# Kernel tuning notes

Measured on AMD Instinct MI355X. Metric: run time of the kernel, lower is better.

The kernel has to match this reference:

```python
import jax, jax.numpy as jnp
import numpy as np

B, LO, LQ = 4, 2048, 2048
NIN, H, G, NH = 41, 128, 10, 2


def _lin(key, din, dout):
    kw, kb = jax.random.split(key)
    W = jax.random.normal(kw, (din, dout), jnp.float32) / np.float32(np.sqrt(din))
    b = jax.random.normal(kb, (dout,), jnp.float32) * 0.01
    return W, b


def setup_inputs() -> dict:
    key = jax.random.key(0)
    ks = jax.random.split(key, 24)
    t_obs = jax.random.normal(ks[0], (B, LO, 1), jnp.float32)
    ch_obs = jax.random.randint(ks[1], (B, LO, 1), 0, NIN).astype(jnp.float32)
    v_obs = jax.random.normal(ks[2], (B, LO, 1), jnp.float32)
    obs = jnp.concatenate([t_obs, ch_obs, v_obs], -1)  # [B, LO, 3]
    t_q = jax.random.normal(ks[3], (B, LQ, 1), jnp.float32)
    ch_q = jax.random.randint(ks[4], (B, LQ, 1), 0, NIN).astype(jnp.float32)
    xq = jnp.concatenate([t_q, ch_q], -1)  # [B, LQ, 2]
    mobs = (jax.random.uniform(ks[5], (B, LO)) < 0.9).astype(jnp.float32)
    mq = (jax.random.uniform(ks[6], (B, LQ)) < 0.9).astype(jnp.float32)
    w_q0, b_q0 = _lin(ks[7], 1, 1)
    w_q1, b_q1 = _lin(ks[8], 1, H - 1)
    w_o0, b_o0 = _lin(ks[9], 1, 1)
    w_o1, b_o1 = _lin(ks[10], 1, H - 1)
    w_cobs, b_cobs = _lin(ks[11], NIN, H)
    w_cq, b_cq = _lin(ks[12], NIN, H)
    w_qp, b_qp = _lin(ks[13], 2 * H, H)
    w_kp, b_kp = _lin(ks[14], 2 * H + 1, H)
    ws_q, ws_qb = _lin(ks[15], H, H * NH)
    ws_o, ws_ob = _lin(ks[16], H * NH, H)
    ww_q, ww_qb = _lin(ks[17], H, H * NH)
    ww_o, ww_ob = _lin(ks[18], H * NH, H)
    wc_q, wc_qb = _lin(ks[19], H, H * NH)
    wc_o, wc_ob = _lin(ks[20], H * NH, H)
    w_split, b_split = _lin(ks[21], H, H * G)
    mix_wt = jax.random.normal(ks[22], (G, H), jnp.float32)
    w_mix, b_mix = _lin(ks[23], H, 1)
    return dict(obs=obs, mobs=mobs, xq=xq, mq=mq,
                w_q0=w_q0, b_q0=b_q0, w_q1=w_q1, b_q1=b_q1,
                w_o0=w_o0, b_o0=b_o0, w_o1=w_o1, b_o1=b_o1,
                w_cobs=w_cobs, b_cobs=b_cobs, w_cq=w_cq, b_cq=b_cq,
                w_qp=w_qp, b_qp=b_qp, w_kp=w_kp, b_kp=b_kp,
                ws_q=ws_q, ws_qb=ws_qb, ws_o=ws_o, ws_ob=ws_ob,
                ww_q=ww_q, ww_qb=ww_qb, ww_o=ww_o, ww_ob=ww_ob,
                wc_q=wc_q, wc_qb=wc_qb, wc_o=wc_o, wc_ob=wc_ob,
                w_split=w_split, b_split=b_split,
                mix_wt=mix_wt, w_mix=w_mix, b_mix=b_mix)


def _mha(q_in, k_in, v_in, mask, Wq, bq, Wo, bo):
    # Faithful to original: query_param projects q, k AND v (key/val params are unused).
    Bb, Lq, _ = q_in.shape
    Lk = k_in.shape[1]
    q = (q_in @ Wq + bq).reshape(Bb, Lq, NH, H)
    k = (k_in @ Wq + bq).reshape(Bb, Lk, NH, H)
    v = (v_in @ Wq + bq).reshape(Bb, Lk, NH, H)
    scores = jnp.einsum('bqhd,bkhd->bhqk', q, k) / np.float32(np.sqrt(H))
    scores = jnp.where(mask[:, None, :, :] == 0, jnp.float32(-1e6), scores)
    attn = jax.nn.softmax(scores, axis=-1)
    out = jnp.einsum('bhqk,bkhd->bqhd', attn, v).reshape(Bb, Lq, NH * H)
    return q_in + out @ Wo + bo


def _forward(obs, mobs, xq, mq,
             w_q0, b_q0, w_q1, b_q1, w_o0, b_o0, w_o1, b_o1,
             w_cobs, b_cobs, w_cq, b_cq, w_qp, b_qp, w_kp, b_kp,
             ws_q, ws_qb, ws_o, ws_ob, ww_q, ww_qb, ww_o, ww_ob,
             wc_q, wc_qb, wc_o, wc_ob, w_split, b_split,
             mix_wt, w_mix, b_mix):
    cq = xq[:, :, 1]
    tq = xq[:, :, 0:1]
    cobs = obs[:, :, 1]
    tobs = obs[:, :, 0:1]
    xobs = obs[:, :, 2:]
    tq = jnp.concatenate([tq @ w_q0 + b_q0, jnp.sin(tq @ w_q1 + b_q1)], -1)        # [B, LQ, H]
    tobs = jnp.concatenate([tobs @ w_o0 + b_o0, jnp.sin(tobs @ w_o1 + b_o1)], -1)  # [B, LO, H]
    cobs = jax.nn.one_hot(cobs.astype(jnp.int32), NIN, dtype=obs.dtype)
    cq = jax.nn.one_hot(cq.astype(jnp.int32), NIN, dtype=obs.dtype)
    cobs = jax.nn.relu(cobs @ w_cobs + b_cobs)
    cq = jax.nn.relu(cq @ w_cq + b_cq)
    obs_ = jnp.concatenate([tobs, cobs, xobs], -1) * mobs[:, :, None]  # [B, LO, 2H+1]
    xq_ = jnp.concatenate([tq, cq], -1) * mq[:, :, None]               # [B, LQ, 2H]
    qry_embed = xq_ @ w_qp + b_qp    # [B, LQ, H]
    obs_embed = obs_ @ w_kp + b_kp   # [B, LO, H]
    mask_self = mobs[:, :, None] * mobs[:, None, :]   # [B, LO, LO]
    mask_cross = mq[:, :, None] * mobs[:, None, :]    # [B, LQ, LO]
    mask_wts = jnp.broadcast_to(mobs[:, None, :], (obs.shape[0], G, mobs.shape[1]))  # [B, G, LO]
    wts_query = jnp.broadcast_to(mix_wt[None], (obs.shape[0], G, H))
    x = jax.nn.relu(_mha(obs_embed, obs_embed, obs_embed, mask_self, ws_q, ws_qb, ws_o, ws_ob))
    mw_ = _mha(wts_query, x, x, mask_wts, ww_q, ww_qb, ww_o, ww_ob)
    mw = jax.nn.softmax((mw_ @ w_mix + b_mix)[..., 0], axis=-1)  # [B, G]
    x = jax.nn.relu(_mha(qry_embed, x, x, mask_cross, wc_q, wc_qb, wc_o, wc_ob))
    x = (x @ w_split + b_split).reshape(x.shape[0], x.shape[1], G, H)
    return jnp.transpose(x, (0, 2, 1, 3)), mw  # ([B, G, LQ, H], [B, G])


def reference(obs, mobs, xq, mq,
              w_q0, b_q0, w_q1, b_q1, w_o0, b_o0, w_o1, b_o1,
              w_cobs, b_cobs, w_cq, b_cq, w_qp, b_qp, w_kp, b_kp,
              ws_q, ws_qb, ws_o, ws_ob, ww_q, ww_qb, ww_o, ww_ob,
              wc_q, wc_qb, wc_o, wc_ob, w_split, b_split,
              mix_wt, w_mix, b_mix):
    return _forward(obs, mobs, xq, mq,
                    w_q0, b_q0, w_q1, b_q1, w_o0, b_o0, w_o1, b_o1,
                    w_cobs, b_cobs, w_cq, b_cq, w_qp, b_qp, w_kp, b_kp,
                    ws_q, ws_qb, ws_o, ws_ob, ww_q, ww_qb, ww_o, ww_ob,
                    wc_q, wc_qb, wc_o, wc_ob, w_split, b_split,
                    mix_wt, w_mix, b_mix)
```

## Files before the change

### kernel.cpp

```cpp
#include <hip/hip_runtime.h>
#include <hip/hip_bf16.h>

#define B_  4
#define L_  2048
#define H_  128
#define NH_ 2
#define G_  10
#define NIN_ 41

typedef __hip_bfloat16 bf16;
typedef __attribute__((ext_vector_type(8))) short bf16x8s;
typedef __attribute__((ext_vector_type(4))) float f32x4;

__device__ __forceinline__ unsigned short f2bf_bits(float x) {
    __hip_bfloat16 h = __float2bfloat16(x);
    return *reinterpret_cast<unsigned short*>(&h);
}
__device__ __forceinline__ float us2f(unsigned short s) {
    return __uint_as_float(((unsigned int)s) << 16);
}

__global__ __launch_bounds__(128)
void featall_kernel(const float* __restrict__ xq, const float* __restrict__ mq,
                    const float* __restrict__ obs, const float* __restrict__ mobs,
                    const float* __restrict__ w_q0, const float* __restrict__ b_q0,
                    const float* __restrict__ w_q1, const float* __restrict__ b_q1,
                    const float* __restrict__ w_cq, const float* __restrict__ b_cq,
                    const float* __restrict__ w_o0, const float* __restrict__ b_o0,
                    const float* __restrict__ w_o1, const float* __restrict__ b_o1,
                    const float* __restrict__ w_cobs, const float* __restrict__ b_cobs,
                    bf16* __restrict__ featq, bf16* __restrict__ feato)
{
    const int blk = blockIdx.x;
    const int j   = threadIdx.x;
    const int NROW = B_ * L_;
    if (blk < NROW) {
        const int row = blk;
        const float t   = xq[row * 2 + 0];
        const float chf = xq[row * 2 + 1];
        int ch = (int)chf; ch = max(0, min(NIN_ - 1, ch));
        const float m   = mq[row];
        float tf;
        if (j == 0) tf = t * w_q0[0] + b_q0[0];
        else        tf = __sinf(t * w_q1[j - 1] + b_q1[j - 1]);
        float cf = fmaxf(w_cq[ch * H_ + j] + b_cq[j], 0.f);
        featq[(size_t)row * 256 + j]       = __float2bfloat16(tf * m);
        featq[(size_t)row * 256 + 128 + j] = __float2bfloat16(cf * m);
    } else {
        const int row = blk - NROW;
        const float t   = obs[row * 3 + 0];
        const float chf = obs[row * 3 + 1];
        const float xv  = obs[row * 3 + 2];
        int ch = (int)chf; ch = max(0, min(NIN_ - 1, ch));
        const float m   = mobs[row];
        float tf;
        if (j == 0) tf = t * w_o0[0] + b_o0[0];
        else        tf = __sinf(t * w_o1[j - 1] + b_o1[j - 1]);
        float cf = fmaxf(w_cobs[ch * H_ + j] + b_cobs[j], 0.f);
        bf16* r = feato + (size_t)row * 288;
        r[j]       = __float2bfloat16(tf * m);
        r[128 + j] = __float2bfloat16(cf * m);
        if (j == 0) r[256] = __float2bfloat16(xv * m);
        if (j < 31) r[257 + j] = __float2bfloat16(0.f);
    }
}

struct WtArgs {
    const float* W[8];
    bf16* T[8];
    int K[8], Kp[8], N[8];
};
__global__ __launch_bounds__(288)
void wtrans_all_kernel(WtArgs a)
{
    const int i = blockIdx.y, n = blockIdx.x, k = threadIdx.x;
    if (n >= a.N[i] || k >= a.Kp[i]) return;
    a.T[i][(size_t)n * a.Kp[i] + k] =
        (k < a.K[i]) ? __float2bfloat16(a.W[i][(size_t)k * a.N[i] + n])
                     : __float2bfloat16(0.f);
}

__global__ __launch_bounds__(256)
void kvtrans_kernel(const bf16* __restrict__ in, bf16* __restrict__ out)
{
    __shared__ unsigned short tile[64 * 136];
    const int tid = threadIdx.x;
    const int l0 = blockIdx.x * 64;
    const int bh = blockIdx.y;
    const unsigned short* src = (const unsigned short*)(in + (size_t)bh * L_ * H_);
    unsigned short* dst = (unsigned short*)(out + (size_t)bh * H_ * L_);
    #pragma unroll
    for (int p = 0; p < 4; p++) {
        const int l = p * 16 + (tid >> 4);
        const int d0 = (tid & 15) * 8;
        *(uint4*)&tile[l * 136 + d0] = *(const uint4*)&src[(size_t)(l0 + l) * H_ + d0];
    }
    __syncthreads();
    const int d  = tid >> 1;
    const int lh = (tid & 1) * 32;
    unsigned short buf[32];
    #pragma unroll
    for (int j = 0; j < 32; j++) buf[j] = tile[(lh + j) * 136 + d];
    #pragma unroll
    for (int j = 0; j < 4; j++)
        *(uint4*)&dst[(size_t)d * L_ + l0 + lh + j * 8] = *(uint4*)&buf[j * 8];
}

__global__ __launch_bounds__(128)
void gemm_kernel(const bf16* __restrict__ A, const bf16* __restrict__ WT,
                 const float* __restrict__ bias, const bf16* __restrict__ R,
                 void* __restrict__ out, int K, int N, int mode, int do_relu)
{
    const int wave = threadIdx.x >> 6, lane = threadIdx.x & 63;
    const int quad = lane >> 4, l15 = lane & 15;
    const int m0 = blockIdx.x * 32 + wave * 16;
    const int n0 = blockIdx.y * 64;

    f32x4 acc[4];
    #pragma unroll
    for (int c = 0; c < 4; c++) acc[c] = (f32x4){0.f, 0.f, 0.f, 0.f};

    const bf16* arow = A + (size_t)(m0 + l15) * K;
    #pragma unroll 4
    for (int kc = 0; kc < K; kc += 32) {
        bf16x8s af = *(const bf16x8s*)(arow + kc + quad * 8);
        #pragma unroll
        for (int c = 0; c < 4; c++) {
            bf16x8s wf = *(const bf16x8s*)(WT + (size_t)(n0 + c * 16 + l15) * K + kc + quad * 8);
            acc[c] = __builtin_amdgcn_mfma_f32_16x16x32_bf16(af, wf, acc[c], 0, 0, 0);
        }
    }

    #pragma unroll
    for (int c = 0; c < 4; c++) {
        const int n = n0 + c * 16 + l15;
        const float bv = bias[n];
        #pragma unroll
        for (int r = 0; r < 4; r++) {
            const int m = m0 + quad * 4 + r;
            float v = acc[c][r] + bv;
            if (R != nullptr) v += __bfloat162float(R[(size_t)m * N + n]);
            if (do_relu) v = fmaxf(v, 0.f);
            if (mode == 0) {
                ((float*)out)[(size_t)m * N + n] = v;
            } else if (mode == 1) {
                ((bf16*)out)[(size_t)m * N + n] = __float2bfloat16(v);
            } else if (mode == 2) {
                const int b = m >> 11, l = m & 2047, hh = n >> 7, d = n & 127;
                ((bf16*)out)[(((size_t)(b * NH_ + hh)) * L_ + l) * H_ + d] = __float2bfloat16(v);
            } else {
                const int b = m >> 11, q = m & 2047, g = n >> 7, hh = n & 127;
                ((float*)out)[(((size_t)(b * G_ + g)) * L_ + q) * H_ + hh] = v;
            }
        }
    }
}

#define KT_S 136
#define VT_S 72
#define PS_S 72

__global__ __launch_bounds__(512, 2)
void flash_attn_kernel(const bf16* __restrict__ Qb, const bf16* __restrict__ KVb,
                       const bf16* __restrict__ KVTb,
                       const float* __restrict__ mQ, const float* __restrict__ mK,
                       bf16* __restrict__ O)
{
    __shared__ __align__(16) char smem[90112];
    unsigned short* Ks = (unsigned short*)smem;
    unsigned short* Vs = (unsigned short*)(smem + 34816);
    unsigned short* Ps = (unsigned short*)(smem + 71680);
    float* Ocomb = (float*)smem;
    float* mcomb = (float*)(smem + 33792);
    float* lcomb = (float*)(smem + 34048);

    const int tid  = threadIdx.x;
    const int lane = tid & 63;
    const int wave = tid >> 6;
    const int half = wave >> 2;
    const int wq   = wave & 3;
    const int quad = lane >> 4;
    const int l15  = lane & 15;
    const int t256 = tid & 255;
    const int bh = blockIdx.x, b = bh >> 1, h = bh & 1;
    const int q0 = blockIdx.y * 64;

    const bf16* kvb = KVb  + (size_t)bh * L_ * H_;
    const bf16* kvt = KVTb + (size_t)bh * H_ * L_;
    const float* mkb = mK + b * L_;

    const bf16* qrow = Qb + ((size_t)bh * L_ + q0 + wq * 16 + l15) * H_;
    bf16x8s qf[4];
    #pragma unroll
    for (int kc = 0; kc < 4; kc++)
        qf[kc] = *(const bf16x8s*)(qrow + kc * 32 + quad * 8);

    bool qz[4];
    #pragma unroll
    for (int r = 0; r < 4; r++)
        qz[r] = (mQ != nullptr) && (mQ[b * L_ + q0 + wq * 16 + quad * 4 + r] == 0.f);

    float mo[4], li[4];
    f32x4 Oacc[8];
    #pragma unroll
    for (int r = 0; r < 4; r++) { mo[r] = -1e30f; li[r] = 0.f; }
    #pragma unroll
    for (int c = 0; c < 8; c++) Oacc[c] = (f32x4){0.f, 0.f, 0.f, 0.f};

    const float SCALE = 0.08838834764831845f;
    unsigned short* KsH = Ks + half * 64 * KT_S;
    unsigned short* VsH = Vs + half * 128 * VT_S;
    unsigned short* pw  = Ps + wave * 16 * PS_S;

    const int krow_b = t256 >> 4, kcol = (t256 & 15) * 8;
    const int vrow_b = t256 >> 3, vcol = (t256 & 7) * 8;

    uint4 rk[4], rv[4];
    const int ks0 = half * 1024;

    {
        const int kb = ks0;
        #pragma unroll
        for (int p = 0; p < 4; p++)
            rk[p] = *(const uint4*)(kvb + (size_t)(kb + p * 16 + krow_b) * H_ + kcol);
        #pragma unroll
        for (int p = 0; p < 4; p++)
            rv[p] = *(const uint4*)(kvt + (size_t)(p * 32 + vrow_b) * L_ + kb + vcol);
        #pragma unroll
        for (int p = 0; p < 4; p++)
            *(uint4*)&KsH[(p * 16 + krow_b) * KT_S + kcol] = rk[p];
        #pragma unroll
        for (int p = 0; p < 4; p++)
            *(uint4*)&VsH[(p * 32 + vrow_b) * VT_S + vcol] = rv[p];
    }
    __syncthreads();

    for (int it = 0; it < 16; it++) {
        const int kb = ks0 + it * 64;

        if (it + 1 < 16) {
            const int kn = kb + 64;
            #pragma unroll
            for (int p = 0; p < 4; p++)
                rk[p] = *(const uint4*)(kvb + (size_t)(kn + p * 16 + krow_b) * H_ + kcol);
            #pragma unroll
            for (int p = 0; p < 4; p++)
                rv[p] = *(const uint4*)(kvt + (size_t)(p * 32 + vrow_b) * L_ + kn + vcol);
        }

        float koff[4];
        #pragma unroll
        for (int t = 0; t < 4; t++)
            koff[t] = (mkb[kb + t * 16 + l15] != 0.f) ? 0.f : -1000000.f;

        f32x4 sa[4];
        #pragma unroll
        for (int t = 0; t < 4; t++) sa[t] = (f32x4){0.f, 0.f, 0.f, 0.f};
        #pragma unroll
        for (int t = 0; t < 4; t++)
            #pragma unroll
            for (int kc = 0; kc < 4; kc++) {
                bf16x8s kf = *(const bf16x8s*)&KsH[(t * 16 + l15) * KT_S + kc * 32 + quad * 8];
                sa[t] = __builtin_amdgcn_mfma_f32_16x16x32_bf16(qf[kc], kf, sa[t], 0, 0, 0);
            }

        float s[4][4], mx[4];
        #pragma unroll
        for (int r = 0; r < 4; r++) {
            #pragma unroll
            for (int t = 0; t < 4; t++) {
                const float v = sa[t][r] * SCALE + koff[t];
                s[t][r] = qz[r] ? -1000000.f : v;
            }
            mx[r] = fmaxf(fmaxf(s[0][r], s[1][r]), fmaxf(s[2][r], s[3][r]));
        }
        #pragma unroll
        for (int off = 1; off < 16; off <<= 1)
            #pragma unroll
            for (int r = 0; r < 4; r++) mx[r] = fmaxf(mx[r], __shfl_xor(mx[r], off));

        float al[4], rs[4];
        #pragma unroll
        for (int r = 0; r < 4; r++) {
            const float mn = fmaxf(mo[r], mx[r]);
            al[r] = __expf(mo[r] - mn);
            mo[r] = mn;
            rs[r] = 0.f;
        }
        #pragma unroll
        for (int t = 0; t < 4; t++)
            #pragma unroll
            for (int r = 0; r < 4; r++) {
                const float p = __expf(s[t][r] - mo[r]);
                rs[r] += p;
                pw[(quad * 4 + r) * PS_S + t * 16 + l15] = f2bf_bits(p);
            }
        #pragma unroll
        for (int off = 1; off < 16; off <<= 1)
            #pragma unroll
            for (int r = 0; r < 4; r++) rs[r] += __shfl_xor(rs[r], off);
        #pragma unroll
        for (int r = 0; r < 4; r++) li[r] = li[r] * al[r] + rs[r];
        #pragma unroll
        for (int c = 0; c < 8; c++)
            #pragma unroll
            for (int r = 0; r < 4; r++) Oacc[c][r] *= al[r];

        bf16x8s pf0 = *(bf16x8s*)&pw[l15 * PS_S + quad * 8];
        bf16x8s pf1 = *(bf16x8s*)&pw[l15 * PS_S + 32 + quad * 8];

        #pragma unroll
        for (int c = 0; c < 8; c++) {
            bf16x8s v0 = *(const bf16x8s*)&VsH[(c * 16 + l15) * VT_S + quad * 8];
            bf16x8s v1 = *(const bf16x8s*)&VsH[(c * 16 + l15) * VT_S + 32 + quad * 8];
            Oacc[c] = __builtin_amdgcn_mfma_f32_16x16x32_bf16(pf0, v0, Oacc[c], 0, 0, 0);
            Oacc[c] = __builtin_amdgcn_mfma_f32_16x16x32_bf16(pf1, v1, Oacc[c], 0, 0, 0);
        }

        __syncthreads();
        if (it + 1 < 16) {
            #pragma unroll
            for (int p = 0; p < 4; p++)
                *(uint4*)&KsH[(p * 16 + krow_b) * KT_S + kcol] = rk[p];
            #pragma unroll
            for (int p = 0; p < 4; p++)
                *(uint4*)&VsH[(p * 32 + vrow_b) * VT_S + vcol] = rv[p];
            __syncthreads();
        }
    }

    if (half == 1) {
        #pragma unroll
        for (int c = 0; c < 8; c++)
            #pragma unroll
            for (int r = 0; r < 4; r++)
                Ocomb[(size_t)(wq * 16 + quad * 4 + r) * 132 + c * 16 + l15] = Oacc[c][r];
        if (l15 == 0) {
            #pragma unroll
            for (int r = 0; r < 4; r++) {
                mcomb[wq * 16 + quad * 4 + r] = mo[r];
                lcomb[wq * 16 + quad * 4 + r] = li[r];
            }
        }
    }
    __syncthreads();
    if (half == 0) {
        bf16* orow = O + ((size_t)b * L_ + q0 + wq * 16) * (NH_ * H_) + h * H_;
        #pragma unroll
        for (int r = 0; r < 4; r++) {
            const int row = quad * 4 + r;
            const float m1 = mcomb[wq * 16 + row];
            const float l1 = lcomb[wq * 16 + row];
            const float M  = fmaxf(mo[r], m1);
            const float a0 = __expf(mo[r] - M);
            const float a1 = __expf(m1 - M);
            const float inv = 1.f / (a0 * li[r] + a1 * l1);
            #pragma unroll
            for (int c = 0; c < 8; c++)
                orow[(size_t)row * (NH_ * H_) + c * 16 + l15] =
                    __float2bfloat16((a0 * Oacc[c][r] +
                                      a1 * Ocomb[(size_t)(wq * 16 + row) * 132 + c * 16 + l15]) * inv);
        }
    }
}

__global__ __launch_bounds__(256)
void qmwb_kernel(const float* __restrict__ mixwt, const float* __restrict__ W,
                 const float* __restrict__ bias, bf16* __restrict__ qmwb)
{
    const int g = blockIdx.x;
    const int c = threadIdx.x;
    const int h = c >> 7, d = c & 127;
    if (g >= G_) { qmwb[((size_t)h * 16 + g) * 128 + d] = __float2bfloat16(0.f); return; }
    __shared__ float xr[128];
    if (c < 128) xr[c] = mixwt[g * 128 + c];
    __syncthreads();
    float acc = bias[c];
    #pragma unroll 8
    for (int i = 0; i < 128; i++)
        acc += xr[i] * W[i * 256 + c];
    qmwb[((size_t)h * 16 + g) * 128 + d] = __float2bfloat16(acc);
}

__global__ __launch_bounds__(256)
void mwpartial_kernel(const bf16* __restrict__ qmwb, const bf16* __restrict__ kvmw,
                      const float* __restrict__ mK,
                      float* __restrict__ mwO, float* __restrict__ mwM,
                      float* __restrict__ mwL)
{
    __shared__ __align__(16) unsigned short Ks[128 * 136];
    __shared__ float Qs[10 * 128];
    __shared__ float sc[10 * 128];
    __shared__ float mst[10], lst[10];

    const int tid = threadIdx.x;
    const int split = blockIdx.x, h = blockIdx.y, b = blockIdx.z;
    const int kbase = split * 128;
    const float SCALE = 0.08838834764831845f;

    for (int idx = tid; idx < 1280; idx += 256)
        Qs[idx] = __bfloat162float(qmwb[((size_t)h * 16 + (idx >> 7)) * 128 + (idx & 127)]);
    {
        const int rr = tid >> 1, half = tid & 1;
        const bf16* src = kvmw + (((size_t)(b * NH_ + h)) * L_ + kbase + rr) * H_ + half * 64;
        #pragma unroll
        for (int i = 0; i < 8; i++)
            *(uint4*)(&Ks[rr * 136 + half * 64 + i * 8]) = *(const uint4*)(src + i * 8);
    }
    __syncthreads();

    {
        const int j = tid & 127, qh = tid >> 7;
        float acc[5] = {0.f, 0.f, 0.f, 0.f, 0.f};
        for (int dc = 0; dc < 128; dc += 8) {
            bf16x8s kv = *(bf16x8s*)(&Ks[j * 136 + dc]);
            float kf[8];
            #pragma unroll
            for (int e = 0; e < 8; e++) kf[e] = us2f(((unsigned short*)&kv)[e]);
            #pragma unroll
            for (int qq = 0; qq < 5; qq++) {
                const float* Qrow = &Qs[(qh * 5 + qq) * 128 + dc];
                #pragma unroll
                for (int e = 0; e < 8; e++) acc[qq] += Qrow[e] * kf[e];
            }
        }
        const bool kz = (mK[b * L_ + kbase + j] == 0.f);
        #pragma unroll
        for (int qq = 0; qq < 5; qq++)
            sc[(qh * 5 + qq) * 128 + j] = kz ? -1000000.f : acc[qq] * SCALE;
    }
    __syncthreads();
    if (tid < 160) {
        const int q = tid >> 4, t16 = tid & 15;
        float m = -3.4e38f;
        for (int jj = t16; jj < 128; jj += 16) m = fmaxf(m, sc[q * 128 + jj]);
        #pragma unroll
        for (int off = 1; off < 16; off <<= 1) m = fmaxf(m, __shfl_xor(m, off));
        if (t16 == 0) mst[q] = m;
    }
    __syncthreads();
    {
        const int j = tid & 127, qh = tid >> 7;
        #pragma unroll
        for (int qq = 0; qq < 5; qq++) {
            const int idx = (qh * 5 + qq) * 128 + j;
            sc[idx] = __expf(sc[idx] - mst[qh * 5 + qq]);
        }
    }
    __syncthreads();
    if (tid < 160) {
        const int q = tid >> 4, t16 = tid & 15;
        float s = 0.f;
        for (int jj = t16; jj < 128; jj += 16) s += sc[q * 128 + jj];
        #pragma unroll
        for (int off = 1; off < 16; off <<= 1) s += __shfl_xor(s, off);
        if (t16 == 0) lst[q] = s;
    }
    __syncthreads();
    {
        const int d = tid & 127, qh = tid >> 7;
        float acc[5] = {0.f, 0.f, 0.f, 0.f, 0.f};
        for (int jj = 0; jj < 128; jj++) {
            const float v = us2f(Ks[jj * 136 + d]);
            #pragma unroll
            for (int qq = 0; qq < 5; qq++)
                acc[qq] += sc[(qh * 5 + qq) * 128 + jj] * v;
        }
        const size_t base = ((size_t)(b * NH_ + h) * 16 + split) * 10;
        #pragma unroll
        for (int qq = 0; qq < 5; qq++)
            mwO[(base + qh * 5 + qq) * 128 + d] = acc[qq];
    }
    if (tid < 10) {
        const size_t base = ((size_t)(b * NH_ + h) * 16 + split) * 10;
        mwM[base + tid] = mst[tid];
        mwL[base + tid] = lst[tid];
    }
}

__global__ __launch_bounds__(256)
void mwcombine_kernel(const float* __restrict__ mwO, const float* __restrict__ mwM,
                      const float* __restrict__ mwL, float* __restrict__ mwat)
{
    const int bg = blockIdx.x;
    const int b = bg / G_, q = bg % G_;
    const int h = threadIdx.x >> 7, d = threadIdx.x & 127;
    const size_t hb = (size_t)(b * NH_ + h) * 16;
    float M = -3.4e38f;
    for (int s = 0; s < 16; s++) M = fmaxf(M, mwM[(hb + s) * 10 + q]);
    float l = 0.f, o = 0.f;
    for (int s = 0; s < 16; s++) {
        const float a = __expf(mwM[(hb + s) * 10 + q] - M);
        l += a * mwL[(hb + s) * 10 + q];
        o += a * mwO[((hb + s) * 10 + q) * 128 + d];
    }
    mwat[(size_t)bg * 256 + h * 128 + d] = o / l;
}

__global__ __launch_bounds__(128)
void mwproj_kernel(const float* __restrict__ A, const float* __restrict__ mixwt,
                   const float* __restrict__ W, const float* __restrict__ bias,
                   float* __restrict__ Y)
{
    const int bg  = blockIdx.x;
    const int g   = bg % G_;
    const int tid = threadIdx.x;
    __shared__ float ar[256];
    ar[tid]       = A[(size_t)bg * 256 + tid];
    ar[tid + 128] = A[(size_t)bg * 256 + tid + 128];
    __syncthreads();
    float acc = mixwt[g * 128 + tid] + bias[tid];
    #pragma unroll 8
    for (int i = 0; i < 256; i++)
        acc += ar[i] * W[i * 128 + tid];
    Y[(size_t)bg * 128 + tid] = acc;
}

__global__ __launch_bounds__(64)
void mwfinal_kernel(const float* __restrict__ MW, const float* __restrict__ wmix,
                    const float* __restrict__ bmix, float* __restrict__ out)
{
    const int b = blockIdx.x;
    const int g = threadIdx.x;
    __shared__ float z[16];
    if (g < G_) {
        float acc = bmix[0];
        for (int i = 0; i < 128; i++)
            acc += MW[((size_t)b * G_ + g) * 128 + i] * wmix[i];
        z[g] = acc;
    }
    __syncthreads();
    if (g == 0) {
        float mx = -3.4e38f;
        for (int i = 0; i < G_; i++) mx = fmaxf(mx, z[i]);
        float e[G_]; float s = 0.f;
        for (int i = 0; i < G_; i++) { e[i] = __expf(z[i] - mx); s += e[i]; }
        for (int i = 0; i < G_; i++) out[b * G_ + i] = e[i] / s;
    }
}

extern "C" void kernel_launch(void* const* d_in, const int* in_sizes, int n_in,
                              void* d_out, int out_size, void* d_ws, size_t ws_size,
                              hipStream_t stream)
{
    const float* obs    = (const float*)d_in[0];
    const float* mobs   = (const float*)d_in[1];
    const float* xq     = (const float*)d_in[2];
    const float* mq     = (const float*)d_in[3];
    const float* w_q0   = (const float*)d_in[4];
    const float* b_q0   = (const float*)d_in[5];
    const float* w_q1   = (const float*)d_in[6];
    const float* b_q1   = (const float*)d_in[7];
    const float* w_o0   = (const float*)d_in[8];
    const float* b_o0   = (const float*)d_in[9];
    const float* w_o1   = (const float*)d_in[10];
    const float* b_o1   = (const float*)d_in[11];
    const float* w_cobs = (const float*)d_in[12];
    const float* b_cobs = (const float*)d_in[13];
    const float* w_cq   = (const float*)d_in[14];
    const float* b_cq   = (const float*)d_in[15];
    const float* w_qp   = (const float*)d_in[16];
    const float* b_qp   = (const float*)d_in[17];
    const float* w_kp   = (const float*)d_in[18];
    const float* b_kp   = (const float*)d_in[19];
    const float* ws_q   = (const float*)d_in[20];
    const float* ws_qb  = (const float*)d_in[21];
    const float* ws_o   = (const float*)d_in[22];
    const float* ws_ob  = (const float*)d_in[23];
    const float* ww_q   = (const float*)d_in[24];
    const float* ww_qb  = (const float*)d_in[25];
    const float* ww_o   = (const float*)d_in[26];
    const float* ww_ob  = (const float*)d_in[27];
    const float* wc_q   = (const float*)d_in[28];
    const float* wc_qb  = (const float*)d_in[29];
    const float* wc_o   = (const float*)d_in[30];
    const float* wc_ob  = (const float*)d_in[31];
    const float* w_split= (const float*)d_in[32];
    const float* b_split= (const float*)d_in[33];
    const float* mix_wt = (const float*)d_in[34];
    const float* w_mix  = (const float*)d_in[35];
    const float* b_mix  = (const float*)d_in[36];

    float* out = (float*)d_out;
    char* ws  = (char*)d_ws;

    const size_t MB = (size_t)1 << 20;
    const size_t KB = (size_t)1 << 10;
    if (ws_size < 31 * MB) return;

    const int NROW = B_ * L_;
    bf16* featq = (bf16*)(ws + 0);
    bf16* feato = (bf16*)(ws + 4 * MB);
    bf16* qe_bf = (bf16*)(ws + 8 * MB + 512 * KB);
    bf16* x_bf  = (bf16*)(ws + 10 * MB + 512 * KB);
    bf16* oe_bf = (bf16*)(ws + 12 * MB + 512 * KB);
    bf16* abuf  = (bf16*)(ws + 14 * MB + 512 * KB);
    bf16* x2_bf = (bf16*)(ws + 18 * MB + 512 * KB);
    bf16* kvmw  = (bf16*)(ws + 20 * MB + 512 * KB);
    bf16* kvT   = (bf16*)(ws + 24 * MB + 512 * KB);
    char* wbase = ws + 28 * MB + 512 * KB;
    bf16* wqpT  = (bf16*)(wbase + 0);
    bf16* wkpT  = (bf16*)(wbase + 64 * KB);
    bf16* wsqT  = (bf16*)(wbase + 136 * KB);
    bf16* wsoT  = (bf16*)(wbase + 200 * KB);
    bf16* wwqT  = (bf16*)(wbase + 264 * KB);
    bf16* wcqT  = (bf16*)(wbase + 328 * KB);
    bf16* wcoT  = (bf16*)(wbase + 392 * KB);
    bf16* wsplT = (bf16*)(wbase + 456 * KB);
    bf16* qmwb  = (bf16*)(wbase + 776 * KB);
    float* mwO  = (float*)(wbase + 784 * KB);
    float* mwM  = (float*)(wbase + 1424 * KB);
    float* mwL  = (float*)(wbase + 1432 * KB);
    float* mwat = (float*)(wbase + 1440 * KB);
    float* mw_  = (float*)(wbase + 1480 * KB);
    bf16* kvbs  = featq;
    bf16* qcb   = featq;
    bf16* kvcb  = (bf16*)(ws + 4 * MB);
    bf16* abuf2 = abuf;

    WtArgs wa;
    wa.W[0]=w_qp;   wa.T[0]=wqpT;  wa.K[0]=256; wa.Kp[0]=256; wa.N[0]=128;
    wa.W[1]=w_kp;   wa.T[1]=wkpT;  wa.K[1]=257; wa.Kp[1]=288; wa.N[1]=128;
    wa.W[2]=ws_q;   wa.T[2]=wsqT;  wa.K[2]=128; wa.Kp[2]=128; wa.N[2]=256;
    wa.W[3]=ws_o;   wa.T[3]=wsoT;  wa.K[3]=256; wa.Kp[3]=256; wa.N[3]=128;
    wa.W[4]=ww_q;   wa.T[4]=wwqT;  wa.K[4]=128; wa.Kp[4]=128; wa.N[4]=256;
    wa.W[5]=wc_q;   wa.T[5]=wcqT;  wa.K[5]=128; wa.Kp[5]=128; wa.N[5]=256;
    wa.W[6]=wc_o;   wa.T[6]=wcoT;  wa.K[6]=256; wa.Kp[6]=256; wa.N[6]=128;
    wa.W[7]=w_split;wa.T[7]=wsplT; wa.K[7]=128; wa.Kp[7]=128; wa.N[7]=1280;
    wtrans_all_kernel<<<dim3(1280, 8), 288, 0, stream>>>(wa);

    featall_kernel<<<2 * NROW, 128, 0, stream>>>(xq, mq, obs, mobs,
                                                 w_q0, b_q0, w_q1, b_q1, w_cq, b_cq,
                                                 w_o0, b_o0, w_o1, b_o1, w_cobs, b_cobs,
                                                 featq, feato);
    gemm_kernel<<<dim3(NROW/32, 2), 128, 0, stream>>>(featq, wqpT, b_qp, nullptr,
                                                      qe_bf, 256, 128, 1, 0);
    gemm_kernel<<<dim3(NROW/32, 2), 128, 0, stream>>>(feato, wkpT, b_kp, nullptr,
                                                      oe_bf, 288, 128, 1, 0);
    gemm_kernel<<<dim3(NROW/32, 4), 128, 0, stream>>>(oe_bf, wsqT, ws_qb, nullptr,
                                                      kvbs, 128, 256, 2, 0);
    kvtrans_kernel<<<dim3(L_/64, B_*NH_), 256, 0, stream>>>(kvbs, kvT);
    flash_attn_kernel<<<dim3(B_*NH_, L_/64), 512, 0, stream>>>(kvbs, kvbs, kvT,
                                                               nullptr, mobs, abuf);
    gemm_kernel<<<dim3(NROW/32, 2), 128, 0, stream>>>(abuf, wsoT, ws_ob, oe_bf,
                                                      x_bf, 256, 128, 1, 1);
    qmwb_kernel<<<16, 256, 0, stream>>>(mix_wt, ww_q, ww_qb, qmwb);
    gemm_kernel<<<dim3(NROW/32, 4), 128, 0, stream>>>(x_bf, wwqT, ww_qb, nullptr,
                                                      kvmw, 128, 256, 2, 0);
    mwpartial_kernel<<<dim3(16, NH_, B_), 256, 0, stream>>>(qmwb, kvmw, mobs,
                                                            mwO, mwM, mwL);
    mwcombine_kernel<<<B_ * G_, 256, 0, stream>>>(mwO, mwM, mwL, mwat);
    mwproj_kernel<<<B_ * G_, 128, 0, stream>>>(mwat, mix_wt, ww_o, ww_ob, mw_);
    mwfinal_kernel<<<B_, 64, 0, stream>>>(mw_, w_mix, b_mix,
                                          out + (size_t)B_ * G_ * L_ * H_);
    gemm_kernel<<<dim3(2*NROW/32, 4), 128, 0, stream>>>(qe_bf, wcqT, wc_qb, nullptr,
                                                        qcb, 128, 256, 2, 0);
    kvtrans_kernel<<<dim3(L_/64, B_*NH_), 256, 0, stream>>>(kvcb, kvT);
    flash_attn_kernel<<<dim3(B_*NH_, L_/64), 512, 0, stream>>>(qcb, kvcb, kvT,
                                                               mq, mobs, abuf2);
    gemm_kernel<<<dim3(NROW/32, 2), 128, 0, stream>>>(abuf2, wcoT, wc_ob, qe_bf,
                                                      x2_bf, 256, 128, 1, 1);
    gemm_kernel<<<dim3(NROW/32, 20), 128, 0, stream>>>(x2_bf, wsplT, b_split, nullptr,
                                                       out, 128, 1280, 3, 0);

    (void)in_sizes; (void)n_in; (void)out_size;
}
```

Baseline: 493.3 us.

## Halve flash-attention query tile and fuse mix-weight tail kernels

The flash attention kernel now processes 32 query rows per block with 4 waves (two key halves by two query groups) instead of 64 rows with 8 waves. That doubles the grid size, and each thread loads twice as many K/V tiles per step. Separately, the three small mix-weight kernels (combine, projection, final softmax) are merged into one per-batch kernel that keeps intermediates in shared memory, removing two launches and global round-trips. The cost is more K/V reloading across blocks and a much less parallel tail kernel (4 blocks).

```diff
diff --git a/kernel.cpp b/kernel.cpp
--- a/kernel.cpp
+++ b/kernel.cpp
@@ -160,30 +160,30 @@
 #define VT_S 72
 #define PS_S 72
 
-__global__ __launch_bounds__(512, 2)
+__global__ __launch_bounds__(256, 2)
 void flash_attn_kernel(const bf16* __restrict__ Qb, const bf16* __restrict__ KVb,
                        const bf16* __restrict__ KVTb,
                        const float* __restrict__ mQ, const float* __restrict__ mK,
                        bf16* __restrict__ O)
 {
-    __shared__ __align__(16) char smem[90112];
+    __shared__ __align__(16) char smem[80896];
     unsigned short* Ks = (unsigned short*)smem;
     unsigned short* Vs = (unsigned short*)(smem + 34816);
     unsigned short* Ps = (unsigned short*)(smem + 71680);
     float* Ocomb = (float*)smem;
-    float* mcomb = (float*)(smem + 33792);
-    float* lcomb = (float*)(smem + 34048);
+    float* mcomb = (float*)(smem + 16896);
+    float* lcomb = (float*)(smem + 17024);
 
     const int tid  = threadIdx.x;
     const int lane = tid & 63;
     const int wave = tid >> 6;
-    const int half = wave >> 2;
-    const int wq   = wave & 3;
+    const int half = wave >> 1;
+    const int wq   = wave & 1;
     const int quad = lane >> 4;
     const int l15  = lane & 15;
-    const int t256 = tid & 255;
+    const int t128 = tid & 127;
     const int bh = blockIdx.x, b = bh >> 1, h = bh & 1;
-    const int q0 = blockIdx.y * 64;
+    const int q0 = blockIdx.y * 32;
 
     const bf16* kvb = KVb  + (size_t)bh * L_ * H_;
     const bf16* kvt = KVTb + (size_t)bh * H_ * L_;
@@ -212,26 +212,26 @@
     unsigned short* VsH = Vs + half * 128 * VT_S;
     unsigned short* pw  = Ps + wave * 16 * PS_S;
 
-    const int krow_b = t256 >> 4, kcol = (t256 & 15) * 8;
-    const int vrow_b = t256 >> 3, vcol = (t256 & 7) * 8;
-
-    uint4 rk[4], rv[4];
+    const int krow_b = t128 >> 4, kcol = (t128 & 15) * 8;
+    const int vrow_b = t128 >> 3, vcol = (t128 & 7) * 8;
+
+    uint4 rk[8], rv[8];
     const int ks0 = half * 1024;
 
     {
         const int kb = ks0;
         #pragma unroll
-        for (int p = 0; p < 4; p++)
-            rk[p] = *(const uint4*)(kvb + (size_t)(kb + p * 16 + krow_b) * H_ + kcol);
-        #pragma unroll
-        for (int p = 0; p < 4; p++)
-            rv[p] = *(const uint4*)(kvt + (size_t)(p * 32 + vrow_b) * L_ + kb + vcol);
-        #pragma unroll
-        for (int p = 0; p < 4; p++)
-            *(uint4*)&KsH[(p * 16 + krow_b) * KT_S + kcol] = rk[p];
-        #pragma unroll
-        for (int p = 0; p < 4; p++)
-            *(uint4*)&VsH[(p * 32 + vrow_b) * VT_S + vcol] = rv[p];
+        for (int p = 0; p < 8; p++)
+            rk[p] = *(const uint4*)(kvb + (size_t)(kb + p * 8 + krow_b) * H_ + kcol);
+        #pragma unroll
+        for (int p = 0; p < 8; p++)
+            rv[p] = *(const uint4*)(kvt + (size_t)(p * 16 + vrow_b) * L_ + kb + vcol);
+        #pragma unroll
+        for (int p = 0; p < 8; p++)
+            *(uint4*)&KsH[(p * 8 + krow_b) * KT_S + kcol] = rk[p];
+        #pragma unroll
+        for (int p = 0; p < 8; p++)
+            *(uint4*)&VsH[(p * 16 + vrow_b) * VT_S + vcol] = rv[p];
     }
     __syncthreads();
 
@@ -241,11 +241,11 @@
         if (it + 1 < 16) {
             const int kn = kb + 64;
             #pragma unroll
-            for (int p = 0; p < 4; p++)
-                rk[p] = *(const uint4*)(kvb + (size_t)(kn + p * 16 + krow_b) * H_ + kcol);
-            #pragma unroll
-            for (int p = 0; p < 4; p++)
-                rv[p] = *(const uint4*)(kvt + (size_t)(p * 32 + vrow_b) * L_ + kn + vcol);
+            for (int p = 0; p < 8; p++)
+                rk[p] = *(const uint4*)(kvb + (size_t)(kn + p * 8 + krow_b) * H_ + kcol);
+            #pragma unroll
+            for (int p = 0; p < 8; p++)
+                rv[p] = *(const uint4*)(kvt + (size_t)(p * 16 + vrow_b) * L_ + kn + vcol);
         }
 
         float koff[4];
@@ -320,11 +320,11 @@
         __syncthreads();
         if (it + 1 < 16) {
             #pragma unroll
-            for (int p = 0; p < 4; p++)
-                *(uint4*)&KsH[(p * 16 + krow_b) * KT_S + kcol] = rk[p];
-            #pragma unroll
-            for (int p = 0; p < 4; p++)
-                *(uint4*)&VsH[(p * 32 + vrow_b) * VT_S + vcol] = rv[p];
+            for (int p = 0; p < 8; p++)
+                *(uint4*)&KsH[(p * 8 + krow_b) * KT_S + kcol] = rk[p];
+            #pragma unroll
+            for (int p = 0; p < 8; p++)
+                *(uint4*)&VsH[(p * 16 + vrow_b) * VT_S + vcol] = rv[p];
             __syncthreads();
         }
     }
@@ -479,62 +479,56 @@
 }
 
 __global__ __launch_bounds__(256)
-void mwcombine_kernel(const float* __restrict__ mwO, const float* __restrict__ mwM,
-                      const float* __restrict__ mwL, float* __restrict__ mwat)
-{
-    const int bg = blockIdx.x;
-    const int b = bg / G_, q = bg % G_;
-    const int h = threadIdx.x >> 7, d = threadIdx.x & 127;
+void mwtail_kernel(const float* __restrict__ mwO, const float* __restrict__ mwM,
+                   const float* __restrict__ mwL, const float* __restrict__ mixwt,
+                   const float* __restrict__ W, const float* __restrict__ bias,
+                   const float* __restrict__ wmix, const float* __restrict__ bmix,
+                   float* __restrict__ out)
+{
+    __shared__ float mwat[10][256];
+    __shared__ float mwq[10][128];
+    __shared__ float zz[10];
+
+    const int b = blockIdx.x, tid = threadIdx.x;
+    const int h = tid >> 7, d = tid & 127;
+
     const size_t hb = (size_t)(b * NH_ + h) * 16;
-    float M = -3.4e38f;
-    for (int s = 0; s < 16; s++) M = fmaxf(M, mwM[(hb + s) * 10 + q]);
-    float l = 0.f, o = 0.f;
-    for (int s = 0; s < 16; s++) {
-        const float a = __expf(mwM[(hb + s) * 10 + q] - M);
-        l += a * mwL[(hb + s) * 10 + q];
-        o += a * mwO[((hb + s) * 10 + q) * 128 + d];
-    }
-    mwat[(size_t)bg * 256 + h * 128 + d] = o / l;
-}
-
-__global__ __launch_bounds__(128)
-void mwproj_kernel(const float* __restrict__ A, const float* __restrict__ mixwt,
-                   const float* __restrict__ W, const float* __restrict__ bias,
-                   float* __restrict__ Y)
-{
-    const int bg  = blockIdx.x;
-    const int g   = bg % G_;
-    const int tid = threadIdx.x;
-    __shared__ float ar[256];
-    ar[tid]       = A[(size_t)bg * 256 + tid];
-    ar[tid + 128] = A[(size_t)bg * 256 + tid + 128];
-    __syncthreads();
-    float acc = mixwt[g * 128 + tid] + bias[tid];
-    #pragma unroll 8
-    for (int i = 0; i < 256; i++)
-        acc += ar[i] * W[i * 128 + tid];
-    Y[(size_t)bg * 128 + tid] = acc;
-}
-
-__global__ __launch_bounds__(64)
-void mwfinal_kernel(const float* __restrict__ MW, const float* __restrict__ wmix,
-                    const float* __restrict__ bmix, float* __restrict__ out)
-{
-    const int b = blockIdx.x;
-    const int g = threadIdx.x;
-    __shared__ float z[16];
-    if (g < G_) {
+    for (int q = 0; q < G_; q++) {
+        float M = -3.4e38f;
+        for (int s = 0; s < 16; s++) M = fmaxf(M, mwM[(hb + s) * 10 + q]);
+        float l = 0.f, o = 0.f;
+        for (int s = 0; s < 16; s++) {
+            const float a = __expf(mwM[(hb + s) * 10 + q] - M);
+            l += a * mwL[(hb + s) * 10 + q];
+            o += a * mwO[((hb + s) * 10 + q) * 128 + d];
+        }
+        mwat[q][h * 128 + d] = o / l;
+    }
+    __syncthreads();
+
+    #pragma unroll
+    for (int j = 0; j < 5; j++) {
+        const int q = h + 2 * j;
+        float acc = mixwt[q * 128 + d] + bias[d];
+        #pragma unroll 8
+        for (int i = 0; i < 256; i++)
+            acc += mwat[q][i] * W[i * 128 + d];
+        mwq[q][d] = acc;
+    }
+    __syncthreads();
+
+    if (tid < G_) {
         float acc = bmix[0];
         for (int i = 0; i < 128; i++)
-            acc += MW[((size_t)b * G_ + g) * 128 + i] * wmix[i];
-        z[g] = acc;
-    }
-    __syncthreads();
-    if (g == 0) {
+            acc += mwq[tid][i] * wmix[i];
+        zz[tid] = acc;
+    }
+    __syncthreads();
+    if (tid == 0) {
         float mx = -3.4e38f;
-        for (int i = 0; i < G_; i++) mx = fmaxf(mx, z[i]);
+        for (int i = 0; i < G_; i++) mx = fmaxf(mx, zz[i]);
         float e[G_]; float s = 0.f;
-        for (int i = 0; i < G_; i++) { e[i] = __expf(z[i] - mx); s += e[i]; }
+        for (int i = 0; i < G_; i++) { e[i] = __expf(zz[i] - mx); s += e[i]; }
         for (int i = 0; i < G_; i++) out[b * G_ + i] = e[i] / s;
     }
 }
@@ -611,8 +605,6 @@
     float* mwO  = (float*)(wbase + 784 * KB);
     float* mwM  = (float*)(wbase + 1424 * KB);
     float* mwL  = (float*)(wbase + 1432 * KB);
-    float* mwat = (float*)(wbase + 1440 * KB);
-    float* mw_  = (float*)(wbase + 1480 * KB);
     bf16* kvbs  = featq;
     bf16* qcb   = featq;
     bf16* kvcb  = (bf16*)(ws + 4 * MB);
@@ -640,7 +632,7 @@
     gemm_kernel<<<dim3(NROW/32, 4), 128, 0, stream>>>(oe_bf, wsqT, ws_qb, nullptr,
                                                       kvbs, 128, 256, 2, 0);
     kvtrans_kernel<<<dim3(L_/64, B_*NH_), 256, 0, stream>>>(kvbs, kvT);
-    flash_attn_kernel<<<dim3(B_*NH_, L_/64), 512, 0, stream>>>(kvbs, kvbs, kvT,
+    flash_attn_kernel<<<dim3(B_*NH_, L_/32), 256, 0, stream>>>(kvbs, kvbs, kvT,
                                                                nullptr, mobs, abuf);
     gemm_kernel<<<dim3(NROW/32, 2), 128, 0, stream>>>(abuf, wsoT, ws_ob, oe_bf,
                                                       x_bf, 256, 128, 1, 1);
@@ -649,14 +641,13 @@
                                                       kvmw, 128, 256, 2, 0);
     mwpartial_kernel<<<dim3(16, NH_, B_), 256, 0, stream>>>(qmwb, kvmw, mobs,
                                                             mwO, mwM, mwL);
-    mwcombine_kernel<<<B_ * G_, 256, 0, stream>>>(mwO, mwM, mwL, mwat);
-    mwproj_kernel<<<B_ * G_, 128, 0, stream>>>(mwat, mix_wt, ww_o, ww_ob, mw_);
-    mwfinal_kernel<<<B_, 64, 0, stream>>>(mw_, w_mix, b_mix,
+    mwtail_kernel<<<B_, 256, 0, stream>>>(mwO, mwM, mwL, mix_wt, ww_o, ww_ob,
+                                          w_mix, b_mix,
                                           out + (size_t)B_ * G_ * L_ * H_);
     gemm_kernel<<<dim3(2*NROW/32, 4), 128, 0, stream>>>(qe_bf, wcqT, wc_qb, nullptr,
                                                         qcb, 128, 256, 2, 0);
     kvtrans_kernel<<<dim3(L_/64, B_*NH_), 256, 0, stream>>>(kvcb, kvT);
-    flash_attn_kernel<<<dim3(B_*NH_, L_/64), 512, 0, stream>>>(qcb, kvcb, kvT,
+    flash_attn_kernel<<<dim3(B_*NH_, L_/32), 256, 0, stream>>>(qcb, kvcb, kvT,
                                                                mq, mobs, abuf2);
     gemm_kernel<<<dim3(NROW/32, 2), 128, 0, stream>>>(abuf2, wcoT, wc_ob, qe_bf,
                                                       x2_bf, 256, 128, 1, 1);
```

New measurement: 656.2 us. +33.0%, slower.
